# Performance work log

Hardware: AMD Instinct MI355X
Metric: run time of the kernel (lower is better)

## Reference

```python
import jax, jax.numpy as jnp
import numpy as np

N_NODES = 50000
N_EDGES = 800000
HIDDEN = 128
EDGE_DIM = 4
N_LAYERS = 4
MLP_HID = 64


def setup_inputs() -> dict:
    key = jax.random.key(0)
    ks = jax.random.split(key, 12)
    inp = {
        "x": jax.random.normal(ks[0], (N_NODES, 1), dtype=jnp.float32),
        "edge_index": jax.random.randint(ks[1], (2, N_EDGES), 0, N_NODES, dtype=jnp.int64),
        "edge_attr": jax.random.normal(ks[2], (N_EDGES, EDGE_DIM), dtype=jnp.float32),
        # embed: Linear(1, HIDDEN)
        "embed_w": jax.random.normal(ks[3], (1, HIDDEN), dtype=jnp.float32) * 0.5,
        "embed_b": jnp.zeros((HIDDEN,), dtype=jnp.float32),
        # per-layer edge MLP: Linear(EDGE_DIM,64) -> ReLU -> Linear(64,1) -> Softplus
        "ew1": jax.random.normal(ks[4], (N_LAYERS, EDGE_DIM, MLP_HID), dtype=jnp.float32) * (1.0 / np.sqrt(EDGE_DIM)),
        "eb1": jnp.zeros((N_LAYERS, MLP_HID), dtype=jnp.float32),
        "ew2": jax.random.normal(ks[5], (N_LAYERS, MLP_HID, 1), dtype=jnp.float32) * (1.0 / np.sqrt(MLP_HID)),
        "eb2": jnp.zeros((N_LAYERS, 1), dtype=jnp.float32),
        # out head: Linear(H,H) -> ReLU -> Linear(H,1)
        "out_w1": jax.random.normal(ks[6], (HIDDEN, HIDDEN), dtype=jnp.float32) * (1.0 / np.sqrt(HIDDEN)),
        "out_b1": jnp.zeros((HIDDEN,), dtype=jnp.float32),
        "out_w2": jax.random.normal(ks[7], (HIDDEN, 1), dtype=jnp.float32) * (1.0 / np.sqrt(HIDDEN)),
        "out_b2": jnp.zeros((1,), dtype=jnp.float32),
    }
    return inp


def reference(x, edge_index, edge_attr, embed_w, embed_b, ew1, eb1, ew2, eb2,
              out_w1, out_b1, out_w2, out_b2):
    n_nodes = x.shape[0]
    src = edge_index[0]  # x_j (source, PyG flow source_to_target)
    dst = edge_index[1]  # x_i (target, aggregation index)

    h = x @ embed_w + embed_b  # [N, H]
    n_layers = ew1.shape[0]
    for l in range(n_layers):
        # edge MLP -> scalar conductivity k_ij per edge, softplus-positive
        hmid = jax.nn.relu(edge_attr @ ew1[l] + eb1[l])       # [E, 64]
        k = jax.nn.softplus(hmid @ ew2[l] + eb2[l])           # [E, 1]
        msg = k * (h[src] - h[dst])                            # [E, H]
        h = jax.ops.segment_sum(msg, dst, num_segments=n_nodes)  # [N, H]

    out = jax.nn.relu(h @ out_w1 + out_b1) @ out_w2 + out_b2  # [N, 1]
    return out
```

## Files before the change

### kernel.cpp

```cpp
#include <hip/hip_runtime.h>
#include <math.h>

#define NN 50000
#define NE 800000
#define HD 128
#define ED 4
#define NL 4
#define MH 64
#define NBIN 196
#define BINCAP 8192
#define CURSTRIDE 16
#define NBF 782
#define NMLPB 3125

__device__ __forceinline__ float softplus_f(float a) {
    return fmaxf(a, 0.0f) + __logf(1.0f + __expf(-fabsf(a)));
}

__device__ __forceinline__ void mlp_layer(
    int l, int t,
    const float* __restrict__ edge_attr,
    const float* __restrict__ ew1, const float* __restrict__ eb1,
    const float* __restrict__ ew2, const float* __restrict__ eb2,
    float* __restrict__ k_all)
{
    if (t >= NE) return;
    const float4 a0 = *reinterpret_cast<const float4*>(edge_attr + (size_t)t * 4);

    const float* __restrict__ W0 = ew1 + (size_t)(l * ED + 0) * MH;
    const float* __restrict__ W1 = ew1 + (size_t)(l * ED + 1) * MH;
    const float* __restrict__ W2 = ew1 + (size_t)(l * ED + 2) * MH;
    const float* __restrict__ W3 = ew1 + (size_t)(l * ED + 3) * MH;
    const float* __restrict__ B1 = eb1 + (size_t)l * MH;
    const float* __restrict__ V2 = ew2 + (size_t)l * MH;

    float p0 = 0.0f, q0 = 0.0f;
    #pragma unroll 4
    for (int j = 0; j < MH; j += 2) {
        {
            const float w0 = W0[j], w1 = W1[j], w2 = W2[j], w3 = W3[j];
            const float b1 = B1[j], v2 = V2[j];
            float m0 = fmaf(a0.x, w0, fmaf(a0.y, w1, fmaf(a0.z, w2, fmaf(a0.w, w3, b1))));
            p0 = fmaf(fmaxf(m0, 0.0f), v2, p0);
        }
        {
            const float w0 = W0[j+1], w1 = W1[j+1], w2 = W2[j+1], w3 = W3[j+1];
            const float b1 = B1[j+1], v2 = V2[j+1];
            float m0 = fmaf(a0.x, w0, fmaf(a0.y, w1, fmaf(a0.z, w2, fmaf(a0.w, w3, b1))));
            q0 = fmaf(fmaxf(m0, 0.0f), v2, q0);
        }
    }
    k_all[(size_t)l * NE + t] = softplus_f(eb2[l] + (p0 + q0));
}

__global__ __launch_bounds__(256) void fill_mlp0_kernel(
    const int* __restrict__ eidx,
    int* __restrict__ gcur,
    int2* __restrict__ gbin,
    const float* __restrict__ edge_attr,
    const float* __restrict__ ew1, const float* __restrict__ eb1,
    const float* __restrict__ ew2, const float* __restrict__ eb2,
    float* __restrict__ k_all)
{
    __shared__ int hist[NBIN];
    __shared__ int base[NBIN];

    if (blockIdx.x < NBF) {
        int tid = threadIdx.x;
        if (tid < NBIN) hist[tid] = 0;
        __syncthreads();

        int e0 = (blockIdx.x * 256 + tid) * 4;
        int bin[4], dloc[4], rank[4];
        int4 srcs, dsts;
        bool act = e0 < NE;
        if (act) {
            srcs = *reinterpret_cast<const int4*>(eidx + e0);
            dsts = *reinterpret_cast<const int4*>(eidx + NE + e0);
            int dd[4] = {dsts.x, dsts.y, dsts.z, dsts.w};
            #pragma unroll
            for (int i = 0; i < 4; ++i) {
                bin[i]  = dd[i] >> 8;
                dloc[i] = dd[i] & 255;
                rank[i] = atomicAdd(&hist[bin[i]], 1);
            }
        }
        __syncthreads();
        if (tid < NBIN && hist[tid]) base[tid] = atomicAdd(&gcur[tid * CURSTRIDE], hist[tid]);
        __syncthreads();
        if (act) {
            int ss[4] = {srcs.x, srcs.y, srcs.z, srcs.w};
            #pragma unroll
            for (int i = 0; i < 4; ++i) {
                int pos = bin[i] * BINCAP + base[bin[i]] + rank[i];
                gbin[pos] = make_int2(ss[i], (dloc[i] << 20) | (e0 + i));
            }
        }
        return;
    }

    int t = (blockIdx.x - NBF) * 256 + threadIdx.x;
    mlp_layer(0, t, edge_attr, ew1, eb1, ew2, eb2, k_all);
}

__global__ __launch_bounds__(256) void csr_mlp123_kernel(
    const int* __restrict__ gcur,
    const int2* __restrict__ gbin,
    int2* __restrict__ gsorted,
    int2* __restrict__ nodeSD,
    const float* __restrict__ edge_attr,
    const float* __restrict__ ew1, const float* __restrict__ eb1,
    const float* __restrict__ ew2, const float* __restrict__ eb2,
    float* __restrict__ k_all)
{
    __shared__ int cnt[256];
    __shared__ int cur[256];
    __shared__ int wsum[4];
    __shared__ int woff[4];

    if (blockIdx.x < NBIN) {
        int b = blockIdx.x;
        int tid = threadIdx.x;
        int lane = tid & 63;
        int wid = tid >> 6;
        int m = gcur[b * CURSTRIDE];
        const int2* src = gbin + (size_t)b * BINCAP;

        cnt[tid] = 0;
        __syncthreads();
        for (int p = tid; p < m; p += 256) {
            int dloc = src[p].y >> 20;
            atomicAdd(&cnt[dloc], 1);
        }
        __syncthreads();
        int v = cnt[tid];
        int xx = v;
        #pragma unroll
        for (int o = 1; o < 64; o <<= 1) {
            int t = __shfl_up(xx, o);
            if (lane >= o) xx += t;
        }
        if (lane == 63) wsum[wid] = xx;
        __syncthreads();
        if (tid == 0) {
            int a = 0;
            #pragma unroll
            for (int w = 0; w < 4; ++w) { woff[w] = a; a += wsum[w]; }
        }
        __syncthreads();
        int excl = xx + woff[wid] - v;
        cur[tid] = excl;
        int n = (b << 8) + tid;
        if (n < NN) nodeSD[n] = make_int2(b * BINCAP + excl, v);
        __syncthreads();
        for (int p = tid; p < m; p += 256) {
            int2 r = src[p];
            int dloc = r.y >> 20;
            int q = atomicAdd(&cur[dloc], 1);
            gsorted[(size_t)b * BINCAP + q] = make_int2(r.x, r.y & 0xFFFFF);
        }
        return;
    }

    int lb = blockIdx.x - NBIN;
    int l  = 1 + lb / NMLPB;
    int t  = (lb - (l - 1) * NMLPB) * 256 + threadIdx.x;
    mlp_layer(l, t, edge_attr, ew1, eb1, ew2, eb2, k_all);
}

__global__ void sgather_kernel(const int2* __restrict__ nodeSD,
                               const int2* __restrict__ gsorted,
                               const float* __restrict__ k_all,
                               int l,
                               const float* __restrict__ s_in,
                               float* __restrict__ s_out) {
    int t = blockIdx.x * 256 + threadIdx.x;
    int n = t >> 4;
    int gl = threadIdx.x & 15;
    if (n >= NN) return;
    int2 sd = nodeSD[n];
    float sk = 0.0f, sks = 0.0f;
    for (int p = gl; p < sd.y; p += 16) {
        int2 r = gsorted[sd.x + p];
        float kk = k_all[(size_t)l * NE + r.y];
        sk += kk;
        sks = fmaf(kk, s_in[r.x], sks);
    }
    #pragma unroll
    for (int m = 1; m < 16; m <<= 1) {
        sk  += __shfl_xor(sk, m);
        sks += __shfl_xor(sks, m);
    }
    if (gl == 0) s_out[n] = fmaf(-sk, s_in[n], sks);
}

__global__ void sgather_head_kernel(const int2* __restrict__ nodeSD,
                                    const int2* __restrict__ gsorted,
                                    const float* __restrict__ k_all,
                                    const float* __restrict__ s_in,
                                    const float* __restrict__ ew,
                                    const float* __restrict__ ow1,
                                    const float* __restrict__ b1,
                                    const float* __restrict__ w2,
                                    const float* __restrict__ b2,
                                    float* __restrict__ out) {
    __shared__ float su[HD], sb1[HD], sw2[HD];
    if (threadIdx.x < HD) {
        int j = threadIdx.x;
        float a = 0.0f;
        #pragma unroll 8
        for (int c = 0; c < HD; ++c) a = fmaf(ew[c], ow1[c * HD + j], a);
        su[j]  = a;
        sb1[j] = b1[j];
        sw2[j] = w2[j];
    }
    __syncthreads();

    int t = blockIdx.x * 256 + threadIdx.x;
    int n = t >> 4;
    int gl = threadIdx.x & 15;
    if (n >= NN) return;
    int2 sd = nodeSD[n];
    float sk = 0.0f, sks = 0.0f;
    for (int p = gl; p < sd.y; p += 16) {
        int2 r = gsorted[sd.x + p];
        float kk = k_all[3 * (size_t)NE + r.y];
        sk += kk;
        sks = fmaf(kk, s_in[r.x], sks);
    }
    #pragma unroll
    for (int m = 1; m < 16; m <<= 1) {
        sk  += __shfl_xor(sk, m);
        sks += __shfl_xor(sks, m);
    }
    float sv = fmaf(-sk, s_in[n], sks);

    float acc = 0.0f;
    #pragma unroll
    for (int jj = 0; jj < 8; ++jj) {
        int j = gl + jj * 16;
        acc = fmaf(fmaxf(fmaf(sv, su[j], sb1[j]), 0.0f), sw2[j], acc);
    }
    #pragma unroll
    for (int m = 1; m < 16; m <<= 1) acc += __shfl_xor(acc, m);
    if (gl == 0) out[n] = acc + b2[0];
}


extern "C" void kernel_launch(void* const* d_in, const int* in_sizes, int n_in,
                              void* d_out, int out_size, void* d_ws, size_t ws_size,
                              hipStream_t stream) {
    const float* x        = (const float*)d_in[0];
    const int*   eidx     = (const int*)d_in[1];
    const float* edge_attr= (const float*)d_in[2];
    const float* embed_w  = (const float*)d_in[3];
    const float* ew1      = (const float*)d_in[5];
    const float* eb1      = (const float*)d_in[6];
    const float* ew2      = (const float*)d_in[7];
    const float* eb2      = (const float*)d_in[8];
    const float* ow1      = (const float*)d_in[9];
    const float* ob1      = (const float*)d_in[10];
    const float* ow2      = (const float*)d_in[11];
    const float* ob2      = (const float*)d_in[12];
    float* out = (float*)d_out;

    char* ws = (char*)d_ws;
    const size_t kbytes  = (size_t)NL * NE * sizeof(float);
    const size_t gbbytes = (size_t)NBIN * BINCAP * sizeof(int2);
    const size_t curbyte = (size_t)NBIN * CURSTRIDE * sizeof(int);
    const size_t sdbytes = (size_t)NN * sizeof(int2);
    const size_t sbytes  = (size_t)NN * sizeof(float);

    size_t off = 0;
    float* k_all   = (float*)(ws + off); off += kbytes;
    int2*  gbin    = (int2*) (ws + off); off += gbbytes;
    int2*  gsorted = (int2*) (ws + off); off += gbbytes;
    int*   gcur    = (int*)  (ws + off); off += curbyte;
    int2*  nodeSD  = (int2*) (ws + off); off += sdbytes;
    float* sA      = (float*)(ws + off); off += sbytes;
    float* sB      = (float*)(ws + off); off += sbytes;

    hipMemsetAsync(gcur, 0, curbyte, stream);

    fill_mlp0_kernel<<<NBF + NMLPB, 256, 0, stream>>>(
        eidx, gcur, gbin, edge_attr, ew1, eb1, ew2, eb2, k_all);

    csr_mlp123_kernel<<<NBIN + 3 * NMLPB, 256, 0, stream>>>(
        gcur, gbin, gsorted, nodeSD, edge_attr, ew1, eb1, ew2, eb2, k_all);

    const int ggrid = (NN * 16 + 255) / 256;
    sgather_kernel<<<ggrid, 256, 0, stream>>>(nodeSD, gsorted, k_all, 0, x,  sA);
    sgather_kernel<<<ggrid, 256, 0, stream>>>(nodeSD, gsorted, k_all, 1, sA, sB);
    sgather_kernel<<<ggrid, 256, 0, stream>>>(nodeSD, gsorted, k_all, 2, sB, sA);
    sgather_head_kernel<<<ggrid, 256, 0, stream>>>(nodeSD, gsorted, k_all, sA,
                                                   embed_w, ow1, ob1, ow2, ob2, out);
}
```

Measured before the change: 124.3 us.

## Compute all four edge MLPs per edge and pre-permute conductivities into CSR order

Each thread now evaluates all four layers' edge MLPs for two edges and writes them as a float4 per edge, splitting the edge range across the two setup kernels. The first gather pass reads k in CSR order and scatters layers 1–3 into CSR-ordered arrays. Later passes then stream k contiguously instead of gathering it by edge id. The sorted src/edge arrays are also split into separate int arrays. This removes the random k gathers and part of the index traffic, at the cost of extra writes in the first gather pass and higher register pressure in the MLP threads.

```diff
diff --git a/kernel.cpp b/kernel.cpp
--- a/kernel.cpp
+++ b/kernel.cpp
@@ -7,60 +7,78 @@
 #define ED 4
 #define NL 4
 #define MH 64
+#define NE2 400000
+#define NEH 200000
 #define NBIN 196
 #define BINCAP 8192
+#define NSTRIDE (NBIN * BINCAP)
 #define CURSTRIDE 16
 #define NBF 782
-#define NMLPB 3125
+#define NMLPE 782
 
 __device__ __forceinline__ float softplus_f(float a) {
     return fmaxf(a, 0.0f) + __logf(1.0f + __expf(-fabsf(a)));
 }
 
-__device__ __forceinline__ void mlp_layer(
-    int l, int t,
+__device__ __forceinline__ void mlp_all4(
+    int part, int t,
     const float* __restrict__ edge_attr,
     const float* __restrict__ ew1, const float* __restrict__ eb1,
     const float* __restrict__ ew2, const float* __restrict__ eb2,
-    float* __restrict__ k_all)
+    float4* __restrict__ k4)
 {
-    if (t >= NE) return;
-    const float4 a0 = *reinterpret_cast<const float4*>(edge_attr + (size_t)t * 4);
-
-    const float* __restrict__ W0 = ew1 + (size_t)(l * ED + 0) * MH;
-    const float* __restrict__ W1 = ew1 + (size_t)(l * ED + 1) * MH;
-    const float* __restrict__ W2 = ew1 + (size_t)(l * ED + 2) * MH;
-    const float* __restrict__ W3 = ew1 + (size_t)(l * ED + 3) * MH;
-    const float* __restrict__ B1 = eb1 + (size_t)l * MH;
-    const float* __restrict__ V2 = ew2 + (size_t)l * MH;
-
-    float p0 = 0.0f, q0 = 0.0f;
-    #pragma unroll 4
-    for (int j = 0; j < MH; j += 2) {
-        {
-            const float w0 = W0[j], w1 = W1[j], w2 = W2[j], w3 = W3[j];
-            const float b1 = B1[j], v2 = V2[j];
-            float m0 = fmaf(a0.x, w0, fmaf(a0.y, w1, fmaf(a0.z, w2, fmaf(a0.w, w3, b1))));
-            p0 = fmaf(fmaxf(m0, 0.0f), v2, p0);
-        }
-        {
-            const float w0 = W0[j+1], w1 = W1[j+1], w2 = W2[j+1], w3 = W3[j+1];
-            const float b1 = B1[j+1], v2 = V2[j+1];
-            float m0 = fmaf(a0.x, w0, fmaf(a0.y, w1, fmaf(a0.z, w2, fmaf(a0.w, w3, b1))));
-            q0 = fmaf(fmaxf(m0, 0.0f), v2, q0);
-        }
-    }
-    k_all[(size_t)l * NE + t] = softplus_f(eb2[l] + (p0 + q0));
-}
-
-__global__ __launch_bounds__(256) void fill_mlp0_kernel(
+    if (t >= NEH) return;
+    const int e0 = part * NE2 + t;
+    const int e1 = e0 + NEH;
+    const float4 a0 = *reinterpret_cast<const float4*>(edge_attr + (size_t)e0 * 4);
+    const float4 a1 = *reinterpret_cast<const float4*>(edge_attr + (size_t)e1 * 4);
+
+    float r0[NL], r1[NL];
+    #pragma unroll
+    for (int l = 0; l < NL; ++l) {
+        const float* __restrict__ W0 = ew1 + (size_t)(l * ED + 0) * MH;
+        const float* __restrict__ W1 = ew1 + (size_t)(l * ED + 1) * MH;
+        const float* __restrict__ W2 = ew1 + (size_t)(l * ED + 2) * MH;
+        const float* __restrict__ W3 = ew1 + (size_t)(l * ED + 3) * MH;
+        const float* __restrict__ B1 = eb1 + (size_t)l * MH;
+        const float* __restrict__ V2 = ew2 + (size_t)l * MH;
+
+        float p0 = 0.0f, q0 = 0.0f, p1 = 0.0f, q1 = 0.0f;
+        #pragma unroll 4
+        for (int j = 0; j < MH; j += 2) {
+            {
+                const float w0 = W0[j], w1 = W1[j], w2 = W2[j], w3 = W3[j];
+                const float b1 = B1[j], v2 = V2[j];
+                float m0 = fmaf(a0.x, w0, fmaf(a0.y, w1, fmaf(a0.z, w2, fmaf(a0.w, w3, b1))));
+                float m1 = fmaf(a1.x, w0, fmaf(a1.y, w1, fmaf(a1.z, w2, fmaf(a1.w, w3, b1))));
+                p0 = fmaf(fmaxf(m0, 0.0f), v2, p0);
+                p1 = fmaf(fmaxf(m1, 0.0f), v2, p1);
+            }
+            {
+                const float w0 = W0[j+1], w1 = W1[j+1], w2 = W2[j+1], w3 = W3[j+1];
+                const float b1 = B1[j+1], v2 = V2[j+1];
+                float m0 = fmaf(a0.x, w0, fmaf(a0.y, w1, fmaf(a0.z, w2, fmaf(a0.w, w3, b1))));
+                float m1 = fmaf(a1.x, w0, fmaf(a1.y, w1, fmaf(a1.z, w2, fmaf(a1.w, w3, b1))));
+                q0 = fmaf(fmaxf(m0, 0.0f), v2, q0);
+                q1 = fmaf(fmaxf(m1, 0.0f), v2, q1);
+            }
+        }
+        const float bb = eb2[l];
+        r0[l] = softplus_f(bb + (p0 + q0));
+        r1[l] = softplus_f(bb + (p1 + q1));
+    }
+    k4[e0] = make_float4(r0[0], r0[1], r0[2], r0[3]);
+    k4[e1] = make_float4(r1[0], r1[1], r1[2], r1[3]);
+}
+
+__global__ __launch_bounds__(256) void fill_mlpA_kernel(
     const int* __restrict__ eidx,
     int* __restrict__ gcur,
     int2* __restrict__ gbin,
     const float* __restrict__ edge_attr,
     const float* __restrict__ ew1, const float* __restrict__ eb1,
     const float* __restrict__ ew2, const float* __restrict__ eb2,
-    float* __restrict__ k_all)
+    float4* __restrict__ k4)
 {
     __shared__ int hist[NBIN];
     __shared__ int base[NBIN];
@@ -100,18 +118,19 @@
     }
 
     int t = (blockIdx.x - NBF) * 256 + threadIdx.x;
-    mlp_layer(0, t, edge_attr, ew1, eb1, ew2, eb2, k_all);
-}
-
-__global__ __launch_bounds__(256) void csr_mlp123_kernel(
+    mlp_all4(0, t, edge_attr, ew1, eb1, ew2, eb2, k4);
+}
+
+__global__ __launch_bounds__(256) void csr_mlpB_kernel(
     const int* __restrict__ gcur,
     const int2* __restrict__ gbin,
-    int2* __restrict__ gsorted,
+    int* __restrict__ gs_src,
+    int* __restrict__ gs_e,
     int2* __restrict__ nodeSD,
     const float* __restrict__ edge_attr,
     const float* __restrict__ ew1, const float* __restrict__ eb1,
     const float* __restrict__ ew2, const float* __restrict__ eb2,
-    float* __restrict__ k_all)
+    float4* __restrict__ k4)
 {
     __shared__ int cnt[256];
     __shared__ int cur[256];
@@ -157,23 +176,24 @@
             int2 r = src[p];
             int dloc = r.y >> 20;
             int q = atomicAdd(&cur[dloc], 1);
-            gsorted[(size_t)b * BINCAP + q] = make_int2(r.x, r.y & 0xFFFFF);
+            gs_src[(size_t)b * BINCAP + q] = r.x;
+            gs_e  [(size_t)b * BINCAP + q] = r.y & 0xFFFFF;
         }
         return;
     }
 
-    int lb = blockIdx.x - NBIN;
-    int l  = 1 + lb / NMLPB;
-    int t  = (lb - (l - 1) * NMLPB) * 256 + threadIdx.x;
-    mlp_layer(l, t, edge_attr, ew1, eb1, ew2, eb2, k_all);
-}
-
-__global__ void sgather_kernel(const int2* __restrict__ nodeSD,
-                               const int2* __restrict__ gsorted,
-                               const float* __restrict__ k_all,
-                               int l,
-                               const float* __restrict__ s_in,
-                               float* __restrict__ s_out) {
+    int t = (blockIdx.x - NBIN) * 256 + threadIdx.x;
+    mlp_all4(1, t, edge_attr, ew1, eb1, ew2, eb2, k4);
+}
+
+__global__ void sg0_kperm_kernel(const int2* __restrict__ nodeSD,
+                                 const int* __restrict__ gs_src,
+                                 const int* __restrict__ gs_e,
+                                 const float4* __restrict__ k4,
+                                 const float* __restrict__ x,
+                                 float* __restrict__ s_out,
+                                 float* __restrict__ kc)
+{
     int t = blockIdx.x * 256 + threadIdx.x;
     int n = t >> 4;
     int gl = threadIdx.x & 15;
@@ -181,29 +201,60 @@
     int2 sd = nodeSD[n];
     float sk = 0.0f, sks = 0.0f;
     for (int p = gl; p < sd.y; p += 16) {
-        int2 r = gsorted[sd.x + p];
-        float kk = k_all[(size_t)l * NE + r.y];
-        sk += kk;
-        sks = fmaf(kk, s_in[r.x], sks);
+        int pos = sd.x + p;
+        int e = gs_e[pos];
+        int s = gs_src[pos];
+        float4 kv = k4[e];
+        kc[pos]               = kv.y;
+        kc[NSTRIDE + pos]     = kv.z;
+        kc[2 * NSTRIDE + pos] = kv.w;
+        sk += kv.x;
+        sks = fmaf(kv.x, x[s], sks);
     }
     #pragma unroll
     for (int m = 1; m < 16; m <<= 1) {
         sk  += __shfl_xor(sk, m);
         sks += __shfl_xor(sks, m);
     }
+    if (gl == 0) s_out[n] = fmaf(-sk, x[n], sks);
+}
+
+__global__ void sg_stream_kernel(const int2* __restrict__ nodeSD,
+                                 const int* __restrict__ gs_src,
+                                 const float* __restrict__ kcl,
+                                 const float* __restrict__ s_in,
+                                 float* __restrict__ s_out) {
+    int t = blockIdx.x * 256 + threadIdx.x;
+    int n = t >> 4;
+    int gl = threadIdx.x & 15;
+    if (n >= NN) return;
+    int2 sd = nodeSD[n];
+    float sk = 0.0f, sks = 0.0f;
+    for (int p = gl; p < sd.y; p += 16) {
+        int pos = sd.x + p;
+        float kk = kcl[pos];
+        int s = gs_src[pos];
+        sk += kk;
+        sks = fmaf(kk, s_in[s], sks);
+    }
+    #pragma unroll
+    for (int m = 1; m < 16; m <<= 1) {
+        sk  += __shfl_xor(sk, m);
+        sks += __shfl_xor(sks, m);
+    }
     if (gl == 0) s_out[n] = fmaf(-sk, s_in[n], sks);
 }
 
-__global__ void sgather_head_kernel(const int2* __restrict__ nodeSD,
-                                    const int2* __restrict__ gsorted,
-                                    const float* __restrict__ k_all,
-                                    const float* __restrict__ s_in,
-                                    const float* __restrict__ ew,
-                                    const float* __restrict__ ow1,
-                                    const float* __restrict__ b1,
-                                    const float* __restrict__ w2,
-                                    const float* __restrict__ b2,
-                                    float* __restrict__ out) {
+__global__ void sg_head_kernel(const int2* __restrict__ nodeSD,
+                               const int* __restrict__ gs_src,
+                               const float* __restrict__ kcl,
+                               const float* __restrict__ s_in,
+                               const float* __restrict__ ew,
+                               const float* __restrict__ ow1,
+                               const float* __restrict__ b1,
+                               const float* __restrict__ w2,
+                               const float* __restrict__ b2,
+                               float* __restrict__ out) {
     __shared__ float su[HD], sb1[HD], sw2[HD];
     if (threadIdx.x < HD) {
         int j = threadIdx.x;
@@ -223,10 +274,11 @@
     int2 sd = nodeSD[n];
     float sk = 0.0f, sks = 0.0f;
     for (int p = gl; p < sd.y; p += 16) {
-        int2 r = gsorted[sd.x + p];
-        float kk = k_all[3 * (size_t)NE + r.y];
+        int pos = sd.x + p;
+        float kk = kcl[pos];
+        int s = gs_src[pos];
         sk += kk;
-        sks = fmaf(kk, s_in[r.x], sks);
+        sks = fmaf(kk, s_in[s], sks);
     }
     #pragma unroll
     for (int m = 1; m < 16; m <<= 1) {
@@ -265,33 +317,41 @@
     float* out = (float*)d_out;
 
     char* ws = (char*)d_ws;
-    const size_t kbytes  = (size_t)NL * NE * sizeof(float);
+    const size_t k4bytes = (size_t)NE * sizeof(float4);
     const size_t gbbytes = (size_t)NBIN * BINCAP * sizeof(int2);
+    const size_t gsbytes = (size_t)NSTRIDE * sizeof(int);
+    const size_t kcbytes = (size_t)3 * NSTRIDE * sizeof(float);
     const size_t curbyte = (size_t)NBIN * CURSTRIDE * sizeof(int);
     const size_t sdbytes = (size_t)NN * sizeof(int2);
     const size_t sbytes  = (size_t)NN * sizeof(float);
 
     size_t off = 0;
-    float* k_all   = (float*)(ws + off); off += kbytes;
-    int2*  gbin    = (int2*) (ws + off); off += gbbytes;
-    int2*  gsorted = (int2*) (ws + off); off += gbbytes;
-    int*   gcur    = (int*)  (ws + off); off += curbyte;
-    int2*  nodeSD  = (int2*) (ws + off); off += sdbytes;
-    float* sA      = (float*)(ws + off); off += sbytes;
-    float* sB      = (float*)(ws + off); off += sbytes;
+    float4* k4     = (float4*)(ws + off); off += k4bytes;
+    int2*   gbin   = (int2*)  (ws + off); off += gbbytes;
+    int*    gs_src = (int*)   (ws + off); off += gsbytes;
+    int*    gs_e   = (int*)   (ws + off); off += gsbytes;
+    float*  kc     = (float*) (ws + off); off += kcbytes;
+    int*    gcur   = (int*)   (ws + off); off += curbyte;
+    int2*   nodeSD = (int2*)  (ws + off); off += sdbytes;
+    float*  sA     = (float*) (ws + off); off += sbytes;
+    float*  sB     = (float*) (ws + off); off += sbytes;
 
     hipMemsetAsync(gcur, 0, curbyte, stream);
 
-    fill_mlp0_kernel<<<NBF + NMLPB, 256, 0, stream>>>(
-        eidx, gcur, gbin, edge_attr, ew1, eb1, ew2, eb2, k_all);
-
-    csr_mlp123_kernel<<<NBIN + 3 * NMLPB, 256, 0, stream>>>(
-        gcur, gbin, gsorted, nodeSD, edge_attr, ew1, eb1, ew2, eb2, k_all);
+    fill_mlpA_kernel<<<NBF + NMLPE, 256, 0, stream>>>(
+        eidx, gcur, gbin, edge_attr, ew1, eb1, ew2, eb2, k4);
+
+    csr_mlpB_kernel<<<NBIN + NMLPE, 256, 0, stream>>>(
+        gcur, gbin, gs_src, gs_e, nodeSD, edge_attr, ew1, eb1, ew2, eb2, k4);
 
     const int ggrid = (NN * 16 + 255) / 256;
-    sgather_kernel<<<ggrid, 256, 0, stream>>>(nodeSD, gsorted, k_all, 0, x,  sA);
-    sgather_kernel<<<ggrid, 256, 0, stream>>>(nodeSD, gsorted, k_all, 1, sA, sB);
-    sgather_kernel<<<ggrid, 256, 0, stream>>>(nodeSD, gsorted, k_all, 2, sB, sA);
-    sgather_head_kernel<<<ggrid, 256, 0, stream>>>(nodeSD, gsorted, k_all, sA,
-                                                   embed_w, ow1, ob1, ow2, ob2, out);
-}
+    sg0_kperm_kernel<<<ggrid, 256, 0, stream>>>(
+        nodeSD, gs_src, gs_e, k4, x, sA, kc);
+    sg_stream_kernel<<<ggrid, 256, 0, stream>>>(
+        nodeSD, gs_src, kc, sA, sB);
+    sg_stream_kernel<<<ggrid, 256, 0, stream>>>(
+        nodeSD, gs_src, kc + NSTRIDE, sB, sA);
+    sg_head_kernel<<<ggrid, 256, 0, stream>>>(
+        nodeSD, gs_src, kc + 2 * (size_t)NSTRIDE, sA,
+        embed_w, ow1, ob1, ow2, ob2, out);
+}
```

Result: faster. 117.4 us (-5.6%).
